# Optimization experiments

Measured on AMD Instinct MI355X. Metric: run time of the kernel, lower is better.

Reference implementation:

```python
import jax, jax.numpy as jnp
import numpy as np

N, E, IN_DIM, H, C, ED = 100000, 1600000, 128, 8, 16, 16
LN_EPS = 1e-5


def setup_inputs() -> dict:
    key = jax.random.key(0)
    ks = jax.random.split(key, 12)
    s_in = 1.0 / np.sqrt(IN_DIM)
    s_ed = 1.0 / np.sqrt(ED)
    return {
        "edge_index": jax.random.randint(ks[0], (2, E), 0, N, dtype=jnp.int64),
        "point_attr": jax.random.normal(ks[1], (N, IN_DIM), dtype=jnp.float32),
        "edge_attr": jax.random.normal(ks[2], (E, ED), dtype=jnp.float32),
        "W": jax.random.normal(ks[3], (IN_DIM, H * C), dtype=jnp.float32) * s_in,
        "att_src": jax.random.normal(ks[4], (1, H, C), dtype=jnp.float32) * 0.1,
        "att_dst": jax.random.normal(ks[5], (1, H, C), dtype=jnp.float32) * 0.1,
        "W_edge": jax.random.normal(ks[6], (ED, H * C), dtype=jnp.float32) * s_ed,
        "att_edge": jax.random.normal(ks[7], (1, H, C), dtype=jnp.float32) * 0.1,
        "bias": jnp.zeros((H * C,), dtype=jnp.float32),
        "ln_node_g": jnp.ones((H * C,), dtype=jnp.float32),
        "ln_node_b": jnp.zeros((H * C,), dtype=jnp.float32),
        "ln_edge_g": jnp.ones((H,), dtype=jnp.float32),
        "ln_edge_b": jnp.zeros((H,), dtype=jnp.float32),
        "edge_w": jax.random.normal(ks[8], (H, 1), dtype=jnp.float32) / np.sqrt(H),
        "edge_b": jnp.zeros((1,), dtype=jnp.float32),
    }


def _layer_norm(x, g, b):
    mu = jnp.mean(x, axis=-1, keepdims=True)
    var = jnp.mean((x - mu) ** 2, axis=-1, keepdims=True)
    return (x - mu) * jax.lax.rsqrt(var + LN_EPS) * g + b


def reference(edge_index, point_attr, edge_attr, W, att_src, att_dst, W_edge,
              att_edge, bias, ln_node_g, ln_node_b, ln_edge_g, ln_edge_b,
              edge_w, edge_b):
    src, dst = edge_index[0], edge_index[1]
    x = (point_attr @ W).reshape(N, H, C)                 # [N,H,C]
    a_src = jnp.sum(x * att_src, axis=-1)                 # [N,H]
    a_dst = jnp.sum(x * att_dst, axis=-1)                 # [N,H]
    e = (edge_attr @ W_edge).reshape(E, H, C)             # [E,H,C]
    a_edge = jnp.sum(e * att_edge, axis=-1)               # [E,H]
    alpha = jax.nn.leaky_relu(a_src[src] + a_dst[dst] + a_edge, 0.2)
    # segment softmax over destination neighborhoods
    m = jax.ops.segment_max(alpha, dst, num_segments=N)
    m = jnp.where(jnp.isfinite(m), m, 0.0)
    ex = jnp.exp(alpha - m[dst])
    den = jax.ops.segment_sum(ex, dst, num_segments=N)
    alpha_n = ex / (den[dst] + 1e-16)                     # [E,H]
    msg = x[src] * alpha_n[..., None]                     # [E,H,C]
    out = jax.ops.segment_sum(msg, dst, num_segments=N).reshape(N, H * C) + bias
    node_out = jax.nn.leaky_relu(_layer_norm(out, ln_node_g, ln_node_b), 0.01)
    edge_h = _layer_norm(alpha_n, ln_edge_g, ln_edge_b)
    edge_out = jax.nn.relu(edge_h @ edge_w + edge_b)[:, 0]  # [E]
    return node_out, edge_out
```

## Files before the change

kernel.cpp:

```cpp
#include <hip/hip_runtime.h>
#include <hip/hip_bf16.h>

#define NN 100000
#define EE 1600000
#define LN_EPS 1e-5f

__device__ __forceinline__ float bf_lo(unsigned u) {
  union { unsigned i; float f; } c; c.i = u << 16; return c.f;
}
__device__ __forceinline__ float bf_hi(unsigned u) {
  union { unsigned i; float f; } c; c.i = u & 0xffff0000u; return c.f;
}
__device__ __forceinline__ float us_bf(unsigned short u) {
  union { unsigned i; float f; } c; c.i = ((unsigned)u) << 16; return c.f;
}
__device__ __forceinline__ unsigned short f2bf(float f) {
  union { float f; unsigned i; } c; c.f = f;
  unsigned b = c.i + 0x7fffu + ((c.i >> 16) & 1u);
  return (unsigned short)(b >> 16);
}
__device__ __forceinline__ float lrelu02(float v) { return v >= 0.f ? v : 0.2f * v; }

__global__ void k_detect(const void* __restrict__ ei, int* __restrict__ flag) {
  if (threadIdx.x == 0 && blockIdx.x == 0) {
    const unsigned long long* p = (const unsigned long long*)ei;
    int ok = 1;
    for (int i = 0; i < 256; ++i)
      if (p[i] >= (unsigned long long)NN) { ok = 0; break; }
    *flag = ok;
  }
}

__global__ __launch_bounds__(512) void k_gemm_node(
    const float* __restrict__ P, const float* __restrict__ W,
    const float* __restrict__ attS, const float* __restrict__ attD,
    unsigned* __restrict__ xb, unsigned short* __restrict__ a_srcb,
    unsigned short* __restrict__ a_dstb, int nrows) {
  __shared__ float Rl[32 * 66];
  int t = threadIdx.x;
  int w = __builtin_amdgcn_readfirstlane(t >> 6);
  int l = t & 63;
  int rb = blockIdx.x * 64;
  int cb = w * 16;
  float acc[16];
#pragma unroll
  for (int j = 0; j < 16; ++j) acc[j] = 0.f;

  for (int kc = 0; kc < 4; ++kc) {
    __syncthreads();
    {
      int row = t >> 3;
      int k0 = (t & 7) * 4;
      int grow = rb + row;
      float4 v = make_float4(0.f, 0.f, 0.f, 0.f);
      if (grow < nrows)
        v = *(const float4*)(P + (size_t)grow * 128 + kc * 32 + k0);
      Rl[(k0 + 0) * 66 + row] = v.x;
      Rl[(k0 + 1) * 66 + row] = v.y;
      Rl[(k0 + 2) * 66 + row] = v.z;
      Rl[(k0 + 3) * 66 + row] = v.w;
    }
    __syncthreads();
    const float* Wp = W + (size_t)(kc * 32) * 128 + cb;
#pragma unroll 8
    for (int k = 0; k < 32; ++k) {
      float rv = Rl[k * 66 + l];
#pragma unroll
      for (int j = 0; j < 16; ++j) acc[j] = fmaf(rv, Wp[k * 128 + j], acc[j]);
    }
  }
  int row = rb + l;
  if (row < nrows) {
    float sa = 0.f, sd = 0.f;
#pragma unroll
    for (int j = 0; j < 16; ++j) {
      sa = fmaf(acc[j], attS[cb + j], sa);
      sd = fmaf(acc[j], attD[cb + j], sd);
    }
    a_srcb[(size_t)row * 8 + w] = f2bf(sa);
    a_dstb[(size_t)row * 8 + w] = f2bf(sd);
    unsigned pk[8];
#pragma unroll
    for (int m = 0; m < 8; ++m)
      pk[m] = (unsigned)f2bf(acc[2 * m]) | ((unsigned)f2bf(acc[2 * m + 1]) << 16);
    unsigned* xo = xb + (size_t)row * 64 + cb / 2;
    *(uint4*)(xo) = make_uint4(pk[0], pk[1], pk[2], pk[3]);
    *(uint4*)(xo + 4) = make_uint4(pk[4], pk[5], pk[6], pk[7]);
  }
}

__global__ __launch_bounds__(256) void k_convert_prep(
    const void* __restrict__ ei, const int* __restrict__ flag,
    const float* __restrict__ EA, const float* __restrict__ Wedge,
    const float* __restrict__ attE, const unsigned short* __restrict__ a_srcb,
    const unsigned short* __restrict__ a_dstb, int* __restrict__ idx32,
    int* __restrict__ counts, int* __restrict__ rank,
    unsigned* __restrict__ wb) {
  __shared__ float M[16][8];
  int t = threadIdx.x;
  if (t < 128) {
    int d = t >> 3, h = t & 7;
    float s = 0.f;
#pragma unroll
    for (int c = 0; c < 16; ++c)
      s = fmaf(Wedge[d * 128 + h * 16 + c], attE[h * 16 + c], s);
    M[d][h] = s;
  }
  __syncthreads();
  int stride = gridDim.x * 256;
  int i64 = *flag;
#pragma unroll 1
  for (int e = blockIdx.x * 256 + t; e < EE; e += stride) {
    int sv, dv;
    if (i64) {
      sv = (int)((const long long*)ei)[e];
      dv = (int)((const long long*)ei)[EE + e];
    } else {
      sv = ((const int*)ei)[e];
      dv = ((const int*)ei)[EE + e];
    }
    idx32[e] = sv;
    idx32[EE + e] = dv;
    int rk = atomicAdd(&counts[(unsigned)dv * 16], 1);
    uint4 as4 = *(const uint4*)(a_srcb + (unsigned)sv * 8);
    uint4 ad4 = *(const uint4*)(a_dstb + (unsigned)dv * 8);
    const float4* ea4 = (const float4*)(EA + (size_t)e * 16);
    float s0 = 0.f, s1 = 0.f, s2 = 0.f, s3 = 0.f;
    float s4 = 0.f, s5 = 0.f, s6 = 0.f, s7 = 0.f;
#pragma unroll
    for (int i = 0; i < 4; ++i) {
      float4 v = ea4[i];
      const float* Mr = &M[i * 4][0];
      s0 = fmaf(v.x, Mr[0], s0); s1 = fmaf(v.x, Mr[1], s1);
      s2 = fmaf(v.x, Mr[2], s2); s3 = fmaf(v.x, Mr[3], s3);
      s4 = fmaf(v.x, Mr[4], s4); s5 = fmaf(v.x, Mr[5], s5);
      s6 = fmaf(v.x, Mr[6], s6); s7 = fmaf(v.x, Mr[7], s7);
      s0 = fmaf(v.y, Mr[8], s0); s1 = fmaf(v.y, Mr[9], s1);
      s2 = fmaf(v.y, Mr[10], s2); s3 = fmaf(v.y, Mr[11], s3);
      s4 = fmaf(v.y, Mr[12], s4); s5 = fmaf(v.y, Mr[13], s5);
      s6 = fmaf(v.y, Mr[14], s6); s7 = fmaf(v.y, Mr[15], s7);
      s0 = fmaf(v.z, Mr[16], s0); s1 = fmaf(v.z, Mr[17], s1);
      s2 = fmaf(v.z, Mr[18], s2); s3 = fmaf(v.z, Mr[19], s3);
      s4 = fmaf(v.z, Mr[20], s4); s5 = fmaf(v.z, Mr[21], s5);
      s6 = fmaf(v.z, Mr[22], s6); s7 = fmaf(v.z, Mr[23], s7);
      s0 = fmaf(v.w, Mr[24], s0); s1 = fmaf(v.w, Mr[25], s1);
      s2 = fmaf(v.w, Mr[26], s2); s3 = fmaf(v.w, Mr[27], s3);
      s4 = fmaf(v.w, Mr[28], s4); s5 = fmaf(v.w, Mr[29], s5);
      s6 = fmaf(v.w, Mr[30], s6); s7 = fmaf(v.w, Mr[31], s7);
    }
    s0 += bf_lo(as4.x) + bf_lo(ad4.x);
    s1 += bf_hi(as4.x) + bf_hi(ad4.x);
    s2 += bf_lo(as4.y) + bf_lo(ad4.y);
    s3 += bf_hi(as4.y) + bf_hi(ad4.y);
    s4 += bf_lo(as4.z) + bf_lo(ad4.z);
    s5 += bf_hi(as4.z) + bf_hi(ad4.z);
    s6 += bf_lo(as4.w) + bf_lo(ad4.w);
    s7 += bf_hi(as4.w) + bf_hi(ad4.w);
    unsigned pk0 = (unsigned)f2bf(__expf(lrelu02(s0))) |
                   ((unsigned)f2bf(__expf(lrelu02(s1))) << 16);
    unsigned pk1 = (unsigned)f2bf(__expf(lrelu02(s2))) |
                   ((unsigned)f2bf(__expf(lrelu02(s3))) << 16);
    unsigned pk2 = (unsigned)f2bf(__expf(lrelu02(s4))) |
                   ((unsigned)f2bf(__expf(lrelu02(s5))) << 16);
    unsigned pk3 = (unsigned)f2bf(__expf(lrelu02(s6))) |
                   ((unsigned)f2bf(__expf(lrelu02(s7))) << 16);
    rank[e] = rk;
    *(uint4*)(wb + (size_t)e * 4) = make_uint4(pk0, pk1, pk2, pk3);
  }
}

__global__ __launch_bounds__(256) void k_blocksum(const int* __restrict__ counts,
                                                  int* __restrict__ partials, int n) {
  __shared__ int sm[256];
  int t = threadIdx.x;
  int gid = blockIdx.x * 256 + t;
  sm[t] = gid < n ? counts[(unsigned)gid * 16] : 0;
  __syncthreads();
  for (int s = 128; s > 0; s >>= 1) {
    if (t < s) sm[t] += sm[t + s];
    __syncthreads();
  }
  if (t == 0) partials[blockIdx.x] = sm[0];
}

__global__ __launch_bounds__(512) void k_scanpartials(int* __restrict__ partials, int nb) {
  __shared__ int sm[512];
  int t = threadIdx.x;
  int v = t < nb ? partials[t] : 0;
  sm[t] = v;
  __syncthreads();
  for (int off = 1; off < 512; off <<= 1) {
    int u = (t >= off) ? sm[t - off] : 0;
    __syncthreads();
    sm[t] += u;
    __syncthreads();
  }
  if (t < nb) partials[t] = sm[t] - v;
}

__global__ __launch_bounds__(256) void k_scanfinal(const int* __restrict__ counts,
                                                   const int* __restrict__ partials,
                                                   int* __restrict__ offsets, int n) {
  __shared__ int sm[256];
  int t = threadIdx.x;
  int gid = blockIdx.x * 256 + t;
  int v = gid < n ? counts[(unsigned)gid * 16] : 0;
  sm[t] = v;
  __syncthreads();
  for (int off = 1; off < 256; off <<= 1) {
    int u = (t >= off) ? sm[t - off] : 0;
    __syncthreads();
    sm[t] += u;
    __syncthreads();
  }
  int excl = partials[blockIdx.x] + sm[t] - v;
  if (gid < n) offsets[gid] = excl;
  if (gid == n - 1) offsets[n] = excl + v;
}

__global__ __launch_bounds__(256) void k_scatter(
    const int* __restrict__ src, const int* __restrict__ dst,
    const int* __restrict__ rank, const int* __restrict__ offsets,
    const unsigned* __restrict__ wb, unsigned* __restrict__ rec) {
  int stride = gridDim.x * 256;
#pragma unroll 1
  for (int e = blockIdx.x * 256 + threadIdx.x; e < EE; e += stride) {
    int sv = src[e], dv = dst[e], rk = rank[e];
    int off = offsets[dv];
    uint4 w4 = *(const uint4*)(wb + (size_t)e * 4);
    unsigned pos = (unsigned)(off + rk);
    unsigned* rp = rec + (size_t)pos * 8;
    *(uint4*)(rp) = w4;
    *(uint4*)(rp + 4) = make_uint4((unsigned)sv, (unsigned)e, (unsigned)dv, 0u);
  }
}

__global__ __launch_bounds__(512) void k_megaagg(
    const int* __restrict__ offsets, const unsigned* __restrict__ rec,
    const unsigned* __restrict__ xb, const float* __restrict__ bias,
    const float* __restrict__ g, const float* __restrict__ b,
    const float* __restrict__ eg, const float* __restrict__ ebv_,
    const float* __restrict__ ew, const float* __restrict__ ebias,
    float* __restrict__ node_out, float* __restrict__ edge_out) {
  int w = threadIdx.x >> 6, l = threadIdx.x & 63;
  int n = blockIdx.x * 8 + w;
  if (n >= NN) return;
  int s = offsets[n], e = offsets[n + 1];
  int qt = l >> 4, ql = l & 15;
  int h = ql >> 1;
  float dn0 = 0.f, dn1 = 0.f, dn2 = 0.f, dn3 = 0.f;
  float acc[8] = {0.f, 0.f, 0.f, 0.f, 0.f, 0.f, 0.f, 0.f};
  int i = s + qt;
  for (; i + 12 < e; i += 16) {
    const unsigned short* rA = (const unsigned short*)(rec + (unsigned)i * 8u);
    const unsigned short* rB = (const unsigned short*)(rec + (unsigned)(i + 4) * 8u);
    const unsigned short* rC = (const unsigned short*)(rec + (unsigned)(i + 8) * 8u);
    const unsigned short* rD = (const unsigned short*)(rec + (unsigned)(i + 12) * 8u);
    float wA = us_bf(rA[h]); unsigned svA = ((const unsigned*)rA)[4];
    float wB = us_bf(rB[h]); unsigned svB = ((const unsigned*)rB)[4];
    float wC = us_bf(rC[h]); unsigned svC = ((const unsigned*)rC)[4];
    float wD = us_bf(rD[h]); unsigned svD = ((const unsigned*)rD)[4];
    uint4 xA = *(const uint4*)(xb + svA * 64u + (unsigned)(ql * 4));
    uint4 xB = *(const uint4*)(xb + svB * 64u + (unsigned)(ql * 4));
    uint4 xC = *(const uint4*)(xb + svC * 64u + (unsigned)(ql * 4));
    uint4 xD = *(const uint4*)(xb + svD * 64u + (unsigned)(ql * 4));
    dn0 += wA; dn1 += wB; dn2 += wC; dn3 += wD;
    acc[0] = fmaf(wA, bf_lo(xA.x), acc[0]); acc[1] = fmaf(wA, bf_hi(xA.x), acc[1]);
    acc[2] = fmaf(wA, bf_lo(xA.y), acc[2]); acc[3] = fmaf(wA, bf_hi(xA.y), acc[3]);
    acc[4] = fmaf(wA, bf_lo(xA.z), acc[4]); acc[5] = fmaf(wA, bf_hi(xA.z), acc[5]);
    acc[6] = fmaf(wA, bf_lo(xA.w), acc[6]); acc[7] = fmaf(wA, bf_hi(xA.w), acc[7]);
    acc[0] = fmaf(wB, bf_lo(xB.x), acc[0]); acc[1] = fmaf(wB, bf_hi(xB.x), acc[1]);
    acc[2] = fmaf(wB, bf_lo(xB.y), acc[2]); acc[3] = fmaf(wB, bf_hi(xB.y), acc[3]);
    acc[4] = fmaf(wB, bf_lo(xB.z), acc[4]); acc[5] = fmaf(wB, bf_hi(xB.z), acc[5]);
    acc[6] = fmaf(wB, bf_lo(xB.w), acc[6]); acc[7] = fmaf(wB, bf_hi(xB.w), acc[7]);
    acc[0] = fmaf(wC, bf_lo(xC.x), acc[0]); acc[1] = fmaf(wC, bf_hi(xC.x), acc[1]);
    acc[2] = fmaf(wC, bf_lo(xC.y), acc[2]); acc[3] = fmaf(wC, bf_hi(xC.y), acc[3]);
    acc[4] = fmaf(wC, bf_lo(xC.z), acc[4]); acc[5] = fmaf(wC, bf_hi(xC.z), acc[5]);
    acc[6] = fmaf(wC, bf_lo(xC.w), acc[6]); acc[7] = fmaf(wC, bf_hi(xC.w), acc[7]);
    acc[0] = fmaf(wD, bf_lo(xD.x), acc[0]); acc[1] = fmaf(wD, bf_hi(xD.x), acc[1]);
    acc[2] = fmaf(wD, bf_lo(xD.y), acc[2]); acc[3] = fmaf(wD, bf_hi(xD.y), acc[3]);
    acc[4] = fmaf(wD, bf_lo(xD.z), acc[4]); acc[5] = fmaf(wD, bf_hi(xD.z), acc[5]);
    acc[6] = fmaf(wD, bf_lo(xD.w), acc[6]); acc[7] = fmaf(wD, bf_hi(xD.w), acc[7]);
  }
  for (; i < e; i += 4) {
    const unsigned short* rA = (const unsigned short*)(rec + (unsigned)i * 8u);
    float wA = us_bf(rA[h]); unsigned svA = ((const unsigned*)rA)[4];
    uint4 xA = *(const uint4*)(xb + svA * 64u + (unsigned)(ql * 4));
    dn0 += wA;
    acc[0] = fmaf(wA, bf_lo(xA.x), acc[0]); acc[1] = fmaf(wA, bf_hi(xA.x), acc[1]);
    acc[2] = fmaf(wA, bf_lo(xA.y), acc[2]); acc[3] = fmaf(wA, bf_hi(xA.y), acc[3]);
    acc[4] = fmaf(wA, bf_lo(xA.z), acc[4]); acc[5] = fmaf(wA, bf_hi(xA.z), acc[5]);
    acc[6] = fmaf(wA, bf_lo(xA.w), acc[6]); acc[7] = fmaf(wA, bf_hi(xA.w), acc[7]);
  }
  float den = (dn0 + dn1) + (dn2 + dn3);
  den += __shfl_xor(den, 16);
  den += __shfl_xor(den, 32);
#pragma unroll
  for (int j = 0; j < 8; ++j) {
    acc[j] += __shfl_xor(acc[j], 16);
    acc[j] += __shfl_xor(acc[j], 32);
  }
  float inv = 1.f / (den + 1e-16f);
  int c0 = ql * 8;
  float4 bv0 = *(const float4*)(bias + c0);
  float4 bv1 = *(const float4*)(bias + c0 + 4);
  acc[0] = acc[0] * inv + bv0.x;
  acc[1] = acc[1] * inv + bv0.y;
  acc[2] = acc[2] * inv + bv0.z;
  acc[3] = acc[3] * inv + bv0.w;
  acc[4] = acc[4] * inv + bv1.x;
  acc[5] = acc[5] * inv + bv1.y;
  acc[6] = acc[6] * inv + bv1.z;
  acc[7] = acc[7] * inv + bv1.w;
  float sum = ((acc[0] + acc[1]) + (acc[2] + acc[3])) +
              ((acc[4] + acc[5]) + (acc[6] + acc[7]));
#pragma unroll
  for (int off = 1; off < 64; off <<= 1) sum += __shfl_xor(sum, off);
  float mu = sum * (1.f / 512.f);
  float d[8], ss = 0.f;
#pragma unroll
  for (int j = 0; j < 8; ++j) { d[j] = acc[j] - mu; ss += d[j] * d[j]; }
#pragma unroll
  for (int off = 1; off < 64; off <<= 1) ss += __shfl_xor(ss, off);
  float r = rsqrtf(ss * (1.f / 512.f) + LN_EPS);
  if (qt == 0) {
    float4 gv0 = *(const float4*)(g + c0);
    float4 gv1 = *(const float4*)(g + c0 + 4);
    float4 bb0 = *(const float4*)(b + c0);
    float4 bb1 = *(const float4*)(b + c0 + 4);
    float y[8];
    y[0] = d[0] * r * gv0.x + bb0.x;
    y[1] = d[1] * r * gv0.y + bb0.y;
    y[2] = d[2] * r * gv0.z + bb0.z;
    y[3] = d[3] * r * gv0.w + bb0.w;
    y[4] = d[4] * r * gv1.x + bb1.x;
    y[5] = d[5] * r * gv1.y + bb1.y;
    y[6] = d[6] * r * gv1.z + bb1.z;
    y[7] = d[7] * r * gv1.w + bb1.w;
#pragma unroll
    for (int j = 0; j < 8; ++j) y[j] = y[j] >= 0.f ? y[j] : 0.01f * y[j];
    float* no = node_out + (size_t)n * 128 + c0;
    *(float4*)(no) = make_float4(y[0], y[1], y[2], y[3]);
    *(float4*)(no + 4) = make_float4(y[4], y[5], y[6], y[7]);
  }
  float invs[8];
#pragma unroll
  for (int hh = 0; hh < 8; ++hh) invs[hh] = __shfl(inv, hh * 2);
  float gw[8];
  float bsum = ebias[0];
#pragma unroll
  for (int hh = 0; hh < 8; ++hh) {
    float ewv = ew[hh];
    gw[hh] = eg[hh] * ewv;
    bsum += ebv_[hh] * ewv;
  }
  for (int i2 = s + l; i2 < e; i2 += 64) {
    const unsigned* rp = rec + (unsigned)i2 * 8u;
    uint4 w4 = *(const uint4*)(rp);
    unsigned eidx = rp[5];
    unsigned wu[4] = {w4.x, w4.y, w4.z, w4.w};
    float p[8];
#pragma unroll
    for (int m = 0; m < 4; ++m) {
      p[2 * m] = bf_lo(wu[m]) * invs[2 * m];
      p[2 * m + 1] = bf_hi(wu[m]) * invs[2 * m + 1];
    }
    float pm = 0.f;
#pragma unroll
    for (int hh = 0; hh < 8; ++hh) pm += p[hh];
    pm *= 0.125f;
    float var = 0.f, dot = 0.f;
#pragma unroll
    for (int hh = 0; hh < 8; ++hh) {
      float dd = p[hh] - pm;
      var += dd * dd;
      dot += dd * gw[hh];
    }
    var *= 0.125f;
    float rr = rsqrtf(var + LN_EPS);
    float o = dot * rr + bsum;
    edge_out[eidx] = fmaxf(o, 0.f);
  }
}

extern "C" void kernel_launch(void* const* d_in, const int* in_sizes, int n_in,
                              void* d_out, int out_size, void* d_ws, size_t ws_size,
                              hipStream_t stream) {
  const void* edge_index = d_in[0];
  const float* point_attr = (const float*)d_in[1];
  const float* edge_attr = (const float*)d_in[2];
  const float* W = (const float*)d_in[3];
  const float* att_src = (const float*)d_in[4];
  const float* att_dst = (const float*)d_in[5];
  const float* W_edge = (const float*)d_in[6];
  const float* att_edge = (const float*)d_in[7];
  const float* bias = (const float*)d_in[8];
  const float* ln_node_g = (const float*)d_in[9];
  const float* ln_node_b = (const float*)d_in[10];
  const float* ln_edge_g = (const float*)d_in[11];
  const float* ln_edge_b = (const float*)d_in[12];
  const float* edge_w = (const float*)d_in[13];
  const float* edge_b = (const float*)d_in[14];

  char* wsb = (char*)d_ws;
  size_t o = 0;
  auto take = [&](size_t bytes) -> void* {
    void* p = wsb + o;
    o += (bytes + 255) & ~(size_t)255;
    return p;
  };
  int* flag = (int*)take(4);
  int* idx32 = (int*)take((size_t)2 * EE * 4);
  unsigned* xb = (unsigned*)take((size_t)NN * 128 * 2);
  unsigned short* a_srcb = (unsigned short*)take((size_t)NN * 8 * 2);
  unsigned short* a_dstb = (unsigned short*)take((size_t)NN * 8 * 2);
  int* counts = (int*)take((size_t)NN * 16 * 4);
  int* offsets = (int*)take((size_t)(NN + 1) * 4);
  int* rank = (int*)take((size_t)EE * 4);
  int* partials = (int*)take(512 * 4);
  unsigned* wb = (unsigned*)take((size_t)EE * 16);
  unsigned* rec = (unsigned*)take((size_t)EE * 32);

  const int* srcp = idx32;
  const int* dstp = idx32 + EE;
  float* node_out = (float*)d_out;
  float* edge_out = node_out + (size_t)NN * 128;

  int nb_scan = (NN + 255) / 256;

  hipMemsetAsync(counts, 0, (size_t)NN * 16 * 4, stream);

  k_detect<<<1, 64, 0, stream>>>(edge_index, flag);
  k_gemm_node<<<(NN + 63) / 64, 512, 0, stream>>>(point_attr, W, att_src, att_dst,
                                                  xb, a_srcb, a_dstb, NN);
  k_convert_prep<<<2048, 256, 0, stream>>>(edge_index, flag, edge_attr, W_edge,
                                           att_edge, a_srcb, a_dstb, idx32,
                                           counts, rank, wb);
  k_blocksum<<<nb_scan, 256, 0, stream>>>(counts, partials, NN);
  k_scanpartials<<<1, 512, 0, stream>>>(partials, nb_scan);
  k_scanfinal<<<nb_scan, 256, 0, stream>>>(counts, partials, offsets, NN);
  k_scatter<<<2048, 256, 0, stream>>>(srcp, dstp, rank, offsets, wb, rec);
  k_megaagg<<<(NN + 7) / 8, 512, 0, stream>>>(offsets, rec, xb, bias,
                                              ln_node_g, ln_node_b, ln_edge_g,
                                              ln_edge_b, edge_w, edge_b,
                                              node_out, edge_out);
}
```

Measured before the change: 304.8 us.

## Merge node GEMM and edge prep into one interleaved kernel, defer exp to scatter

Fuses the node GEMM and the edge-conversion kernel into a single launch, with even blocks doing the GEMM and odd blocks doing the edge work. This removes the dependency on a_src/a_dst during edge prep so the two phases can run concurrently. The gather of a_src/a_dst, the leaky-relu and the exp move into the scatter kernel, which now does three more gathers per edge. The cost is extra random reads in the scatter, and the edge work is spread over fewer threads (about 1563 blocks of 512 versus 2048 of 256).

```diff
diff --git a/kernel.cpp b/kernel.cpp
--- a/kernel.cpp
+++ b/kernel.cpp
@@ -31,141 +31,126 @@
   }
 }
 
-__global__ __launch_bounds__(512) void k_gemm_node(
+__global__ __launch_bounds__(512) void k_phase1(
     const float* __restrict__ P, const float* __restrict__ W,
     const float* __restrict__ attS, const float* __restrict__ attD,
     unsigned* __restrict__ xb, unsigned short* __restrict__ a_srcb,
-    unsigned short* __restrict__ a_dstb, int nrows) {
-  __shared__ float Rl[32 * 66];
-  int t = threadIdx.x;
-  int w = __builtin_amdgcn_readfirstlane(t >> 6);
-  int l = t & 63;
-  int rb = blockIdx.x * 64;
-  int cb = w * 16;
-  float acc[16];
-#pragma unroll
-  for (int j = 0; j < 16; ++j) acc[j] = 0.f;
-
-  for (int kc = 0; kc < 4; ++kc) {
-    __syncthreads();
-    {
-      int row = t >> 3;
-      int k0 = (t & 7) * 4;
-      int grow = rb + row;
-      float4 v = make_float4(0.f, 0.f, 0.f, 0.f);
-      if (grow < nrows)
-        v = *(const float4*)(P + (size_t)grow * 128 + kc * 32 + k0);
-      Rl[(k0 + 0) * 66 + row] = v.x;
-      Rl[(k0 + 1) * 66 + row] = v.y;
-      Rl[(k0 + 2) * 66 + row] = v.z;
-      Rl[(k0 + 3) * 66 + row] = v.w;
-    }
-    __syncthreads();
-    const float* Wp = W + (size_t)(kc * 32) * 128 + cb;
-#pragma unroll 8
-    for (int k = 0; k < 32; ++k) {
-      float rv = Rl[k * 66 + l];
-#pragma unroll
-      for (int j = 0; j < 16; ++j) acc[j] = fmaf(rv, Wp[k * 128 + j], acc[j]);
-    }
-  }
-  int row = rb + l;
-  if (row < nrows) {
-    float sa = 0.f, sd = 0.f;
-#pragma unroll
-    for (int j = 0; j < 16; ++j) {
-      sa = fmaf(acc[j], attS[cb + j], sa);
-      sd = fmaf(acc[j], attD[cb + j], sd);
-    }
-    a_srcb[(size_t)row * 8 + w] = f2bf(sa);
-    a_dstb[(size_t)row * 8 + w] = f2bf(sd);
-    unsigned pk[8];
-#pragma unroll
-    for (int m = 0; m < 8; ++m)
-      pk[m] = (unsigned)f2bf(acc[2 * m]) | ((unsigned)f2bf(acc[2 * m + 1]) << 16);
-    unsigned* xo = xb + (size_t)row * 64 + cb / 2;
-    *(uint4*)(xo) = make_uint4(pk[0], pk[1], pk[2], pk[3]);
-    *(uint4*)(xo + 4) = make_uint4(pk[4], pk[5], pk[6], pk[7]);
-  }
-}
-
-__global__ __launch_bounds__(256) void k_convert_prep(
+    unsigned short* __restrict__ a_dstb, int nrows,
     const void* __restrict__ ei, const int* __restrict__ flag,
     const float* __restrict__ EA, const float* __restrict__ Wedge,
-    const float* __restrict__ attE, const unsigned short* __restrict__ a_srcb,
-    const unsigned short* __restrict__ a_dstb, int* __restrict__ idx32,
+    const float* __restrict__ attE, int* __restrict__ idx32,
     int* __restrict__ counts, int* __restrict__ rank,
-    unsigned* __restrict__ wb) {
+    unsigned* __restrict__ aedgeb) {
+  __shared__ float Rl[32 * 66];
   __shared__ float M[16][8];
+  int bid = blockIdx.x;
   int t = threadIdx.x;
-  if (t < 128) {
-    int d = t >> 3, h = t & 7;
-    float s = 0.f;
-#pragma unroll
-    for (int c = 0; c < 16; ++c)
-      s = fmaf(Wedge[d * 128 + h * 16 + c], attE[h * 16 + c], s);
-    M[d][h] = s;
-  }
-  __syncthreads();
-  int stride = gridDim.x * 256;
-  int i64 = *flag;
+  if ((bid & 1) == 0) {
+    int w = __builtin_amdgcn_readfirstlane(t >> 6);
+    int l = t & 63;
+    int rb = (bid >> 1) * 64;
+    int cb = w * 16;
+    float acc[16];
+#pragma unroll
+    for (int j = 0; j < 16; ++j) acc[j] = 0.f;
+    for (int kc = 0; kc < 4; ++kc) {
+      __syncthreads();
+      {
+        int row = t >> 3;
+        int k0 = (t & 7) * 4;
+        int grow = rb + row;
+        float4 v = make_float4(0.f, 0.f, 0.f, 0.f);
+        if (grow < nrows)
+          v = *(const float4*)(P + (size_t)grow * 128 + kc * 32 + k0);
+        Rl[(k0 + 0) * 66 + row] = v.x;
+        Rl[(k0 + 1) * 66 + row] = v.y;
+        Rl[(k0 + 2) * 66 + row] = v.z;
+        Rl[(k0 + 3) * 66 + row] = v.w;
+      }
+      __syncthreads();
+      const float* Wp = W + (size_t)(kc * 32) * 128 + cb;
+#pragma unroll 8
+      for (int k = 0; k < 32; ++k) {
+        float rv = Rl[k * 66 + l];
+#pragma unroll
+        for (int j = 0; j < 16; ++j) acc[j] = fmaf(rv, Wp[k * 128 + j], acc[j]);
+      }
+    }
+    int row = rb + l;
+    if (row < nrows) {
+      float sa = 0.f, sd = 0.f;
+#pragma unroll
+      for (int j = 0; j < 16; ++j) {
+        sa = fmaf(acc[j], attS[cb + j], sa);
+        sd = fmaf(acc[j], attD[cb + j], sd);
+      }
+      a_srcb[(size_t)row * 8 + w] = f2bf(sa);
+      a_dstb[(size_t)row * 8 + w] = f2bf(sd);
+      unsigned pk[8];
+#pragma unroll
+      for (int m = 0; m < 8; ++m)
+        pk[m] = (unsigned)f2bf(acc[2 * m]) | ((unsigned)f2bf(acc[2 * m + 1]) << 16);
+      unsigned* xo = xb + (size_t)row * 64 + cb / 2;
+      *(uint4*)(xo) = make_uint4(pk[0], pk[1], pk[2], pk[3]);
+      *(uint4*)(xo + 4) = make_uint4(pk[4], pk[5], pk[6], pk[7]);
+    }
+  } else {
+    if (t < 128) {
+      int d = t >> 3, h = t & 7;
+      float s = 0.f;
+#pragma unroll
+      for (int c = 0; c < 16; ++c)
+        s = fmaf(Wedge[d * 128 + h * 16 + c], attE[h * 16 + c], s);
+      M[d][h] = s;
+    }
+    __syncthreads();
+    int nconv = (int)(gridDim.x >> 1);
+    int stride = nconv * 512;
+    int i64 = *flag;
 #pragma unroll 1
-  for (int e = blockIdx.x * 256 + t; e < EE; e += stride) {
-    int sv, dv;
-    if (i64) {
-      sv = (int)((const long long*)ei)[e];
-      dv = (int)((const long long*)ei)[EE + e];
-    } else {
-      sv = ((const int*)ei)[e];
-      dv = ((const int*)ei)[EE + e];
-    }
-    idx32[e] = sv;
-    idx32[EE + e] = dv;
-    int rk = atomicAdd(&counts[(unsigned)dv * 16], 1);
-    uint4 as4 = *(const uint4*)(a_srcb + (unsigned)sv * 8);
-    uint4 ad4 = *(const uint4*)(a_dstb + (unsigned)dv * 8);
-    const float4* ea4 = (const float4*)(EA + (size_t)e * 16);
-    float s0 = 0.f, s1 = 0.f, s2 = 0.f, s3 = 0.f;
-    float s4 = 0.f, s5 = 0.f, s6 = 0.f, s7 = 0.f;
-#pragma unroll
-    for (int i = 0; i < 4; ++i) {
-      float4 v = ea4[i];
-      const float* Mr = &M[i * 4][0];
-      s0 = fmaf(v.x, Mr[0], s0); s1 = fmaf(v.x, Mr[1], s1);
-      s2 = fmaf(v.x, Mr[2], s2); s3 = fmaf(v.x, Mr[3], s3);
-      s4 = fmaf(v.x, Mr[4], s4); s5 = fmaf(v.x, Mr[5], s5);
-      s6 = fmaf(v.x, Mr[6], s6); s7 = fmaf(v.x, Mr[7], s7);
-      s0 = fmaf(v.y, Mr[8], s0); s1 = fmaf(v.y, Mr[9], s1);
-      s2 = fmaf(v.y, Mr[10], s2); s3 = fmaf(v.y, Mr[11], s3);
-      s4 = fmaf(v.y, Mr[12], s4); s5 = fmaf(v.y, Mr[13], s5);
-      s6 = fmaf(v.y, Mr[14], s6); s7 = fmaf(v.y, Mr[15], s7);
-      s0 = fmaf(v.z, Mr[16], s0); s1 = fmaf(v.z, Mr[17], s1);
-      s2 = fmaf(v.z, Mr[18], s2); s3 = fmaf(v.z, Mr[19], s3);
-      s4 = fmaf(v.z, Mr[20], s4); s5 = fmaf(v.z, Mr[21], s5);
-      s6 = fmaf(v.z, Mr[22], s6); s7 = fmaf(v.z, Mr[23], s7);
-      s0 = fmaf(v.w, Mr[24], s0); s1 = fmaf(v.w, Mr[25], s1);
-      s2 = fmaf(v.w, Mr[26], s2); s3 = fmaf(v.w, Mr[27], s3);
-      s4 = fmaf(v.w, Mr[28], s4); s5 = fmaf(v.w, Mr[29], s5);
-      s6 = fmaf(v.w, Mr[30], s6); s7 = fmaf(v.w, Mr[31], s7);
-    }
-    s0 += bf_lo(as4.x) + bf_lo(ad4.x);
-    s1 += bf_hi(as4.x) + bf_hi(ad4.x);
-    s2 += bf_lo(as4.y) + bf_lo(ad4.y);
-    s3 += bf_hi(as4.y) + bf_hi(ad4.y);
-    s4 += bf_lo(as4.z) + bf_lo(ad4.z);
-    s5 += bf_hi(as4.z) + bf_hi(ad4.z);
-    s6 += bf_lo(as4.w) + bf_lo(ad4.w);
-    s7 += bf_hi(as4.w) + bf_hi(ad4.w);
-    unsigned pk0 = (unsigned)f2bf(__expf(lrelu02(s0))) |
-                   ((unsigned)f2bf(__expf(lrelu02(s1))) << 16);
-    unsigned pk1 = (unsigned)f2bf(__expf(lrelu02(s2))) |
-                   ((unsigned)f2bf(__expf(lrelu02(s3))) << 16);
-    unsigned pk2 = (unsigned)f2bf(__expf(lrelu02(s4))) |
-                   ((unsigned)f2bf(__expf(lrelu02(s5))) << 16);
-    unsigned pk3 = (unsigned)f2bf(__expf(lrelu02(s6))) |
-                   ((unsigned)f2bf(__expf(lrelu02(s7))) << 16);
-    rank[e] = rk;
-    *(uint4*)(wb + (size_t)e * 4) = make_uint4(pk0, pk1, pk2, pk3);
+    for (int e = (bid >> 1) * 512 + t; e < EE; e += stride) {
+      int sv, dv;
+      if (i64) {
+        sv = (int)((const long long*)ei)[e];
+        dv = (int)((const long long*)ei)[EE + e];
+      } else {
+        sv = ((const int*)ei)[e];
+        dv = ((const int*)ei)[EE + e];
+      }
+      idx32[e] = sv;
+      idx32[EE + e] = dv;
+      int rk = atomicAdd(&counts[(unsigned)dv * 16], 1);
+      const float4* ea4 = (const float4*)(EA + (size_t)e * 16);
+      float s0 = 0.f, s1 = 0.f, s2 = 0.f, s3 = 0.f;
+      float s4 = 0.f, s5 = 0.f, s6 = 0.f, s7 = 0.f;
+#pragma unroll
+      for (int i = 0; i < 4; ++i) {
+        float4 v = ea4[i];
+        const float* Mr = &M[i * 4][0];
+        s0 = fmaf(v.x, Mr[0], s0); s1 = fmaf(v.x, Mr[1], s1);
+        s2 = fmaf(v.x, Mr[2], s2); s3 = fmaf(v.x, Mr[3], s3);
+        s4 = fmaf(v.x, Mr[4], s4); s5 = fmaf(v.x, Mr[5], s5);
+        s6 = fmaf(v.x, Mr[6], s6); s7 = fmaf(v.x, Mr[7], s7);
+        s0 = fmaf(v.y, Mr[8], s0); s1 = fmaf(v.y, Mr[9], s1);
+        s2 = fmaf(v.y, Mr[10], s2); s3 = fmaf(v.y, Mr[11], s3);
+        s4 = fmaf(v.y, Mr[12], s4); s5 = fmaf(v.y, Mr[13], s5);
+        s6 = fmaf(v.y, Mr[14], s6); s7 = fmaf(v.y, Mr[15], s7);
+        s0 = fmaf(v.z, Mr[16], s0); s1 = fmaf(v.z, Mr[17], s1);
+        s2 = fmaf(v.z, Mr[18], s2); s3 = fmaf(v.z, Mr[19], s3);
+        s4 = fmaf(v.z, Mr[20], s4); s5 = fmaf(v.z, Mr[21], s5);
+        s6 = fmaf(v.z, Mr[22], s6); s7 = fmaf(v.z, Mr[23], s7);
+        s0 = fmaf(v.w, Mr[24], s0); s1 = fmaf(v.w, Mr[25], s1);
+        s2 = fmaf(v.w, Mr[26], s2); s3 = fmaf(v.w, Mr[27], s3);
+        s4 = fmaf(v.w, Mr[28], s4); s5 = fmaf(v.w, Mr[29], s5);
+        s6 = fmaf(v.w, Mr[30], s6); s7 = fmaf(v.w, Mr[31], s7);
+      }
+      unsigned pk0 = (unsigned)f2bf(s0) | ((unsigned)f2bf(s1) << 16);
+      unsigned pk1 = (unsigned)f2bf(s2) | ((unsigned)f2bf(s3) << 16);
+      unsigned pk2 = (unsigned)f2bf(s4) | ((unsigned)f2bf(s5) << 16);
+      unsigned pk3 = (unsigned)f2bf(s6) | ((unsigned)f2bf(s7) << 16);
+      rank[e] = rk;
+      *(uint4*)(aedgeb + (size_t)e * 4) = make_uint4(pk0, pk1, pk2, pk3);
+    }
   }
 }
 
@@ -218,19 +203,34 @@
   if (gid == n - 1) offsets[n] = excl + v;
 }
 
-__global__ __launch_bounds__(256) void k_scatter(
+__global__ __launch_bounds__(256) void k_wscatter(
     const int* __restrict__ src, const int* __restrict__ dst,
     const int* __restrict__ rank, const int* __restrict__ offsets,
-    const unsigned* __restrict__ wb, unsigned* __restrict__ rec) {
+    const unsigned* __restrict__ aedgeb, const unsigned short* __restrict__ a_srcb,
+    const unsigned short* __restrict__ a_dstb, unsigned* __restrict__ rec) {
   int stride = gridDim.x * 256;
 #pragma unroll 1
   for (int e = blockIdx.x * 256 + threadIdx.x; e < EE; e += stride) {
     int sv = src[e], dv = dst[e], rk = rank[e];
     int off = offsets[dv];
-    uint4 w4 = *(const uint4*)(wb + (size_t)e * 4);
+    uint4 ae4 = *(const uint4*)(aedgeb + (size_t)e * 4);
+    uint4 as4 = *(const uint4*)(a_srcb + (unsigned)sv * 8);
+    uint4 ad4 = *(const uint4*)(a_dstb + (unsigned)dv * 8);
+    unsigned aeu[4] = {ae4.x, ae4.y, ae4.z, ae4.w};
+    unsigned asu[4] = {as4.x, as4.y, as4.z, as4.w};
+    unsigned adu[4] = {ad4.x, ad4.y, ad4.z, ad4.w};
+    unsigned pk[4];
+#pragma unroll
+    for (int m = 0; m < 4; ++m) {
+      float a0 = bf_lo(aeu[m]) + bf_lo(asu[m]) + bf_lo(adu[m]);
+      float a1 = bf_hi(aeu[m]) + bf_hi(asu[m]) + bf_hi(adu[m]);
+      float w0 = __expf(lrelu02(a0));
+      float w1 = __expf(lrelu02(a1));
+      pk[m] = (unsigned)f2bf(w0) | ((unsigned)f2bf(w1) << 16);
+    }
     unsigned pos = (unsigned)(off + rk);
     unsigned* rp = rec + (size_t)pos * 8;
-    *(uint4*)(rp) = w4;
+    *(uint4*)(rp) = make_uint4(pk[0], pk[1], pk[2], pk[3]);
     *(uint4*)(rp + 4) = make_uint4((unsigned)sv, (unsigned)e, (unsigned)dv, 0u);
   }
 }
@@ -418,7 +418,7 @@
   int* offsets = (int*)take((size_t)(NN + 1) * 4);
   int* rank = (int*)take((size_t)EE * 4);
   int* partials = (int*)take(512 * 4);
-  unsigned* wb = (unsigned*)take((size_t)EE * 16);
+  unsigned* aedgeb = (unsigned*)take((size_t)EE * 16);
   unsigned* rec = (unsigned*)take((size_t)EE * 32);
 
   const int* srcp = idx32;
@@ -427,19 +427,20 @@
   float* edge_out = node_out + (size_t)NN * 128;
 
   int nb_scan = (NN + 255) / 256;
+  int ngemm = (NN + 63) / 64;
 
   hipMemsetAsync(counts, 0, (size_t)NN * 16 * 4, stream);
 
   k_detect<<<1, 64, 0, stream>>>(edge_index, flag);
-  k_gemm_node<<<(NN + 63) / 64, 512, 0, stream>>>(point_attr, W, att_src, att_dst,
-                                                  xb, a_srcb, a_dstb, NN);
-  k_convert_prep<<<2048, 256, 0, stream>>>(edge_index, flag, edge_attr, W_edge,
-                                           att_edge, a_srcb, a_dstb, idx32,
-                                           counts, rank, wb);
+  k_phase1<<<2 * ngemm, 512, 0, stream>>>(point_attr, W, att_src, att_dst,
+                                          xb, a_srcb, a_dstb, NN,
+                                          edge_index, flag, edge_attr, W_edge,
+                                          att_edge, idx32, counts, rank, aedgeb);
   k_blocksum<<<nb_scan, 256, 0, stream>>>(counts, partials, NN);
   k_scanpartials<<<1, 512, 0, stream>>>(partials, nb_scan);
   k_scanfinal<<<nb_scan, 256, 0, stream>>>(counts, partials, offsets, NN);
-  k_scatter<<<2048, 256, 0, stream>>>(srcp, dstp, rank, offsets, wb, rec);
+  k_wscatter<<<2048, 256, 0, stream>>>(srcp, dstp, rank, offsets, aedgeb,
+                                       a_srcb, a_dstb, rec);
   k_megaagg<<<(NN + 7) / 8, 512, 0, stream>>>(offsets, rec, xb, bias,
                                               ln_node_g, ln_node_b, ln_edge_g,
                                               ln_edge_b, edge_w, edge_b,
```

Result: slower. 343.3 us (+12.6%).
